# Kernel optimization log

Measured on AMD Instinct MI355X. Metric: run time of the kernel, lower is better.

## Reference

```python
import jax, jax.numpy as jnp
import numpy as np

SCALING = 16.0 / 16  # lora_alpha / rank
INIT_THRESHOLD = 0.01


def setup_inputs() -> dict:
    key = jax.random.key(0)
    k1, k2, k3, k4, k5 = jax.random.split(key, 5)
    B, S, D, R = 4, 2048, 4096, 16
    x = jax.random.normal(k1, (B, S, D), dtype=jnp.float32)
    weight = jax.random.normal(k2, (D, D), dtype=jnp.float32) * (1.0 / np.sqrt(D))
    lora_A = jax.random.normal(k3, (R, D), dtype=jnp.float32) * 0.01
    lora_B = jax.random.normal(k4, (D, R), dtype=jnp.float32) * 0.02
    lora_sigma = jax.random.normal(k5, (R,), dtype=jnp.float32)
    return {"x": x, "weight": weight, "lora_A": lora_A, "lora_B": lora_B,
            "lora_sigma": lora_sigma}


def reference(x, weight, lora_A, lora_B, lora_sigma):
    # mask out singular values below threshold, scale B columns
    mask = (jnp.abs(lora_sigma) >= INIT_THRESHOLD).astype(lora_sigma.dtype)
    sigma_masked = lora_sigma * mask                     # [R]
    # delta = (B * sigma) @ A, scaled; materialized as in original module
    delta = (lora_B * sigma_masked[None, :]) @ lora_A    # [out, in]
    delta = delta * SCALING
    base_out = jnp.einsum('bsd,od->bso', x, weight)      # F.linear(x, W)
    lora_out = jnp.einsum('bsd,od->bso', x, delta)       # dropout p=0 -> identity
    return base_out + lora_out
```

## Files before the change

kernel.cpp:

```cpp
#include <hip/hip_runtime.h>

#define D_DIM 4096
#define R_DIM 16
#define SCALING_F 1.0f
#define THRESH 0.01f

#define BM 128
#define BN 128
#define BK 64

typedef __attribute__((ext_vector_type(8))) short short8;
typedef __attribute__((ext_vector_type(4))) float floatx4;

__device__ __forceinline__ unsigned int f2bf(float f) {
  union { float f; unsigned int u; } v; v.f = f;
  unsigned int u = v.u;
  u += 0x7FFFu + ((u >> 16) & 1u);
  return u >> 16;
}

__global__ __launch_bounds__(256) void convert_x_kernel(
    const float* __restrict__ x, unsigned int* __restrict__ xb, int n8) {
  int idx = blockIdx.x * 256 + threadIdx.x;
  if (idx >= n8) return;
  const float4* xp = (const float4*)x;
  float4 v0 = xp[2 * idx];
  float4 v1 = xp[2 * idx + 1];
  uint4 o;
  o.x = f2bf(v0.x) | (f2bf(v0.y) << 16);
  o.y = f2bf(v0.z) | (f2bf(v0.w) << 16);
  o.z = f2bf(v1.x) | (f2bf(v1.y) << 16);
  o.w = f2bf(v1.z) | (f2bf(v1.w) << 16);
  ((uint4*)xb)[idx] = o;
}

__global__ __launch_bounds__(256) void build_weff_kernel(
    const float* __restrict__ W, const float* __restrict__ lA,
    const float* __restrict__ lB, const float* __restrict__ sigma,
    unsigned int* __restrict__ wb) {
  __shared__ float Bs[R_DIM];
  int idx = blockIdx.x * 256 + threadIdx.x;
  int o  = idx >> 10;
  int dq = idx & 1023;
  if (threadIdx.x < R_DIM) {
    float s = sigma[threadIdx.x];
    s = (fabsf(s) >= THRESH) ? s : 0.0f;
    Bs[threadIdx.x] = lB[o * R_DIM + threadIdx.x] * s * SCALING_F;
  }
  __syncthreads();
  float4 acc = ((const float4*)W)[idx];
#pragma unroll
  for (int r = 0; r < R_DIM; ++r) {
    float b = Bs[r];
    float4 a = ((const float4*)(lA + (size_t)r * D_DIM))[dq];
    acc.x += b * a.x; acc.y += b * a.y; acc.z += b * a.z; acc.w += b * a.w;
  }
  uint2 p;
  p.x = f2bf(acc.x) | (f2bf(acc.y) << 16);
  p.y = f2bf(acc.z) | (f2bf(acc.w) << 16);
  ((uint2*)wb)[idx] = p;
}

__device__ __forceinline__ void load_lds16(const void* g, void* l) {
  __builtin_amdgcn_global_load_lds(
      (const __attribute__((address_space(1))) void*)g,
      (__attribute__((address_space(3))) void*)l, 16, 0, 0);
}

__global__ __launch_bounds__(256) void gemm_bt_kernel(
    const unsigned short* __restrict__ A,
    const unsigned short* __restrict__ B,
    float* __restrict__ C, int M) {
  __shared__ __align__(16) unsigned short sA[BM * BK];
  __shared__ __align__(16) unsigned short sB[BN * BK];

  const int tid  = threadIdx.x;
  const int lane = tid & 63;
  const int wave = tid >> 6;
  const int wm   = wave >> 1;
  const int wn   = wave & 1;
  const int lrow = lane & 15;
  const int lq   = lane >> 4;

  const int m0 = blockIdx.y * BM;
  const int n0 = blockIdx.x * BN;

  floatx4 acc[4][4] = {};

  const int srow = lane >> 3;
  const int kofs = (((lane & 7) ^ srow)) * 8;
  const unsigned short* aG = A + (size_t)(m0 + wave * 32 + srow) * D_DIM + kofs;
  const unsigned short* bG = B + (size_t)(n0 + wave * 32 + srow) * D_DIM + kofs;
  unsigned short* lAc = sA + wave * 2048;
  unsigned short* lBc = sB + wave * 2048;

  const int r7   = lrow & 7;
  const int col0 = (lq ^ r7) * 8;
  const int col1 = ((4 | lq) ^ r7) * 8;
  const int aRow = (wm * 64 + lrow) * BK;
  const int bRow = (wn * 64 + lrow) * BK;

  for (int k0 = 0; k0 < D_DIM; k0 += BK) {
#pragma unroll
    for (int c = 0; c < 4; ++c) {
      load_lds16(aG + (size_t)c * 8 * D_DIM + k0, lAc + c * 512);
      load_lds16(bG + (size_t)c * 8 * D_DIM + k0, lBc + c * 512);
    }
    __syncthreads();

#pragma unroll
    for (int s = 0; s < 2; ++s) {
      const int cs = (s == 0) ? col0 : col1;
      short8 af[4], bf[4];
#pragma unroll
      for (int t = 0; t < 4; ++t) {
        af[t] = *(const short8*)(sA + aRow + t * 16 * BK + cs);
        bf[t] = *(const short8*)(sB + bRow + t * 16 * BK + cs);
      }
#pragma unroll
      for (int i = 0; i < 4; ++i)
#pragma unroll
        for (int j = 0; j < 4; ++j)
          acc[i][j] = __builtin_amdgcn_mfma_f32_16x16x32_bf16(
              af[i], bf[j], acc[i][j], 0, 0, 0);
    }

    __syncthreads();
  }

#pragma unroll
  for (int i = 0; i < 4; ++i) {
    const int row0 = m0 + wm * 64 + i * 16 + lq * 4;
#pragma unroll
    for (int j = 0; j < 4; ++j) {
      const int col = n0 + wn * 64 + j * 16 + lrow;
      float* cp = C + (size_t)row0 * D_DIM + col;
#pragma unroll
      for (int rr = 0; rr < 4; ++rr)
        cp[(size_t)rr * D_DIM] = acc[i][j][rr];
    }
  }
}

extern "C" void kernel_launch(void* const* d_in, const int* in_sizes, int n_in,
                              void* d_out, int out_size, void* d_ws, size_t ws_size,
                              hipStream_t stream) {
  const float* x     = (const float*)d_in[0];
  const float* W     = (const float*)d_in[1];
  const float* lA    = (const float*)d_in[2];
  const float* lB    = (const float*)d_in[3];
  const float* sigma = (const float*)d_in[4];
  float* out = (float*)d_out;

  const int M = in_sizes[0] / D_DIM;
  unsigned int* xb = (unsigned int*)d_ws;
  unsigned int* wb = (unsigned int*)((char*)d_ws + (size_t)M * D_DIM * 2);

  const int n8 = in_sizes[0] / 8;
  convert_x_kernel<<<(n8 + 255) / 256, 256, 0, stream>>>(x, xb, n8);

  const int wquads = (D_DIM * D_DIM) / 4;
  build_weff_kernel<<<wquads / 256, 256, 0, stream>>>(W, lA, lB, sigma, wb);

  dim3 grid(D_DIM / BN, M / BM);
  gemm_bt_kernel<<<grid, 256, 0, stream>>>(
      (const unsigned short*)xb, (const unsigned short*)wb, out, M);
}
```

Measured before the change: 562.5 us.

## Double-buffer LDS tiles to overlap next global load with MFMA compute

Allocates two LDS buffers for the A and B tiles and issues the direct-to-LDS global loads for the next K step before computing on the current one. Partial vmcnt waits plus explicit barriers replace the two __syncthreads per iteration. This is meant to hide global-memory latency behind MFMA work. In exchange it doubles LDS use to 64KB per block, which may lower occupancy, and it depends on hand-written waitcnt counts being correct.

```diff
diff --git a/kernel.cpp b/kernel.cpp
--- a/kernel.cpp
+++ b/kernel.cpp
@@ -71,8 +71,8 @@
     const unsigned short* __restrict__ A,
     const unsigned short* __restrict__ B,
     float* __restrict__ C, int M) {
-  __shared__ __align__(16) unsigned short sA[BM * BK];
-  __shared__ __align__(16) unsigned short sB[BN * BK];
+  __shared__ __align__(16) unsigned short sA[2][BM * BK];
+  __shared__ __align__(16) unsigned short sB[2][BN * BK];
 
   const int tid  = threadIdx.x;
   const int lane = tid & 63;
@@ -91,8 +91,7 @@
   const int kofs = (((lane & 7) ^ srow)) * 8;
   const unsigned short* aG = A + (size_t)(m0 + wave * 32 + srow) * D_DIM + kofs;
   const unsigned short* bG = B + (size_t)(n0 + wave * 32 + srow) * D_DIM + kofs;
-  unsigned short* lAc = sA + wave * 2048;
-  unsigned short* lBc = sB + wave * 2048;
+  const int ldsChunk = wave * 2048;
 
   const int r7   = lrow & 7;
   const int col0 = (lq ^ r7) * 8;
@@ -100,22 +99,37 @@
   const int aRow = (wm * 64 + lrow) * BK;
   const int bRow = (wn * 64 + lrow) * BK;
 
+#pragma unroll
+  for (int c = 0; c < 4; ++c) {
+    load_lds16(aG + (size_t)c * 8 * D_DIM, &sA[0][ldsChunk + c * 512]);
+    load_lds16(bG + (size_t)c * 8 * D_DIM, &sB[0][ldsChunk + c * 512]);
+  }
+
+  int cur = 0;
   for (int k0 = 0; k0 < D_DIM; k0 += BK) {
+    const int kn = k0 + BK;
+    if (kn < D_DIM) {
+      const int nb = cur ^ 1;
 #pragma unroll
-    for (int c = 0; c < 4; ++c) {
-      load_lds16(aG + (size_t)c * 8 * D_DIM + k0, lAc + c * 512);
-      load_lds16(bG + (size_t)c * 8 * D_DIM + k0, lBc + c * 512);
+      for (int c = 0; c < 4; ++c) {
+        load_lds16(aG + kn + (size_t)c * 8 * D_DIM, &sA[nb][ldsChunk + c * 512]);
+        load_lds16(bG + kn + (size_t)c * 8 * D_DIM, &sB[nb][ldsChunk + c * 512]);
+      }
+      asm volatile("s_waitcnt vmcnt(8)\n\ts_barrier" ::: "memory");
+    } else {
+      asm volatile("s_waitcnt vmcnt(0)\n\ts_barrier" ::: "memory");
     }
-    __syncthreads();
 
+    const unsigned short* sAb = sA[cur];
+    const unsigned short* sBb = sB[cur];
 #pragma unroll
     for (int s = 0; s < 2; ++s) {
       const int cs = (s == 0) ? col0 : col1;
       short8 af[4], bf[4];
 #pragma unroll
       for (int t = 0; t < 4; ++t) {
-        af[t] = *(const short8*)(sA + aRow + t * 16 * BK + cs);
-        bf[t] = *(const short8*)(sB + bRow + t * 16 * BK + cs);
+        af[t] = *(const short8*)(sAb + aRow + t * 16 * BK + cs);
+        bf[t] = *(const short8*)(sBb + bRow + t * 16 * BK + cs);
       }
 #pragma unroll
       for (int i = 0; i < 4; ++i)
@@ -125,7 +139,8 @@
               af[i], bf[j], acc[i][j], 0, 0, 0);
     }
 
-    __syncthreads();
+    asm volatile("s_waitcnt lgkmcnt(0)\n\ts_barrier" ::: "memory");
+    cur ^= 1;
   }
 
 #pragma unroll
```

Result: slower. 602.4 us (+7.1%).
